# Kernel optimization log

Measured on AMD Instinct MI355X. Metric: run time of the kernel, lower is better.

## Reference

```python
import jax, jax.numpy as jnp
import numpy as np
import math

SEQ = 45000
FEAT = 30
DEPTH, HEADS, DK, MLP, C = 4, 4, 32, 512, 32
MAXSEQ = 512


def pos_embed_table():
    # Enformer-style basis functions over distances [-SEQ+1, SEQ-1]
    d = jnp.arange(-SEQ + 1, SEQ, dtype=jnp.float32)
    a = jnp.abs(d)[:, None]
    nb = FEAT // 6  # basis per class (exponential / central-mask / gamma)
    # exponential decay
    hl = 2.0 ** jnp.linspace(3.0, math.log(SEQ) / math.log(2.0), nb)
    e1 = jnp.exp(-math.log(2.0) / hl[None, :] * a)
    # central mask
    cw = 2.0 ** jnp.arange(1, nb + 1, dtype=jnp.float32) - 1.0
    e2 = (cw[None, :] > a).astype(jnp.float32)
    # gamma pdf
    stddev = SEQ / (2 * nb)
    start_mean = SEQ / nb
    mean = jnp.linspace(start_mean, float(SEQ), nb)
    conc = (mean / stddev) ** 2
    rate = mean / stddev ** 2
    logp = jax.scipy.special.xlogy(conc - 1.0, a) - rate * a
    logz = jax.scipy.special.gammaln(conc) - conc * jnp.log(rate)
    p = jnp.exp(logp - logz) + 1e-8
    e3 = p / jnp.max(p)
    e = jnp.concatenate([e1, e2, e3], axis=-1)
    return jnp.concatenate([e, jnp.sign(d)[:, None] * e], axis=-1)  # [2*SEQ-1, FEAT]


def layernorm(x, g, b, eps=1e-5):
    mu = jnp.mean(x, axis=-1, keepdims=True)
    var = jnp.var(x, axis=-1, keepdims=True)
    return (x - mu) * jax.lax.rsqrt(var + eps) * g + b


def setup_inputs() -> dict:
    key = jax.random.key(0)
    ks = jax.random.split(key, 16)
    B, L = 2, SEQ
    HD = HEADS * DK
    s = 0.02
    return {
        "x_skip": jax.random.normal(ks[0], (B, C, L), jnp.float32),
        "attention": jax.random.uniform(ks[1], (B, 3, L), jnp.float32),
        "ln1_g": jnp.ones((DEPTH, C), jnp.float32),
        "ln1_b": jnp.zeros((DEPTH, C), jnp.float32),
        "Wq": jax.random.normal(ks[2], (DEPTH, C, HD), jnp.float32) * s,
        "Wk": jax.random.normal(ks[3], (DEPTH, C, HD), jnp.float32) * s,
        "Wv": jax.random.normal(ks[4], (DEPTH, C, HD), jnp.float32) * s,
        "Wrel": jax.random.normal(ks[5], (DEPTH, FEAT, HD), jnp.float32) * s,
        "rcb": jax.random.normal(ks[6], (DEPTH, HEADS, DK), jnp.float32),
        "rpb": jax.random.normal(ks[7], (DEPTH, HEADS, DK), jnp.float32),
        "Wo": jax.random.normal(ks[8], (DEPTH, HD, C), jnp.float32) * s,
        "bo": jnp.zeros((DEPTH, C), jnp.float32),
        "ln2_g": jnp.ones((DEPTH, C), jnp.float32),
        "ln2_b": jnp.zeros((DEPTH, C), jnp.float32),
        "W1": jax.random.normal(ks[9], (DEPTH, C, MLP), jnp.float32) * s,
        "b1": jnp.zeros((DEPTH, MLP), jnp.float32),
        "W2": jax.random.normal(ks[10], (DEPTH, MLP, C), jnp.float32) * s,
        "b2": jnp.zeros((DEPTH, C), jnp.float32),
    }


def reference(x_skip, attention, ln1_g, ln1_b, Wq, Wk, Wv, Wrel, rcb, rpb, Wo, bo, ln2_g, ln2_b, W1, b1, W2, b2):
    B, Cc, L = x_skip.shape
    half = MAXSEQ // 2
    x_emb = jnp.swapaxes(x_skip, 1, 2)  # [B, L, C]
    # top splice sites by acceptor / donor score
    acc = jnp.argsort(-attention[:, 1, :], axis=1)[:, :half]
    don = jnp.argsort(-attention[:, 2, :], axis=1)[:, :half]
    idx = jnp.sort(jnp.concatenate([acc, don], axis=1), axis=1)  # [B, n]
    n = idx.shape[1]
    diff = idx[:, :, None] - idx[:, None, :] + SEQ - 1  # [B, n, n]
    positions = pos_embed_table()[diff]  # [B, n, n, FEAT]
    emb = jnp.take_along_axis(x_emb, idx[:, :, None], axis=1)  # [B, n, C]
    scale = DK ** -0.5
    for l in range(DEPTH):
        h = layernorm(emb, ln1_g[l], ln1_b[l])
        q = (h @ Wq[l]).reshape(B, n, HEADS, DK).transpose(0, 2, 1, 3) * scale
        k = (h @ Wk[l]).reshape(B, n, HEADS, DK).transpose(0, 2, 1, 3)
        v = (h @ Wv[l]).reshape(B, n, HEADS, DK).transpose(0, 2, 1, 3)
        content = jnp.einsum('bhid,bhjd->bhij', q + rcb[l][None, :, None, :], k)
        rel_k = (positions @ Wrel[l]).reshape(B, n, n, HEADS, DK)  # b i j h d
        rel = jnp.einsum('bhid,bijhd->bhij', q + rpb[l][None, :, None, :], rel_k)
        attn_w = jax.nn.softmax(content + rel, axis=-1)
        o = jnp.einsum('bhij,bhjd->bhid', attn_w, v)
        o = o.transpose(0, 2, 1, 3).reshape(B, n, HEADS * DK)
        emb = emb + o @ Wo[l] + bo[l]
        h2 = layernorm(emb, ln2_g[l], ln2_b[l])
        emb = emb + jax.nn.gelu(h2 @ W1[l] + b1[l], approximate=False) @ W2[l] + b2[l]
    out = jnp.zeros_like(x_emb).at[jnp.arange(B)[:, None], idx].set(emb)
    return jnp.swapaxes(out, 1, 2)  # [B, C, L]
```

## Files before the change

kernel.cpp:

```cpp
#include <hip/hip_runtime.h>
#include <math.h>

#define SEQL   45000
#define NBAT   2
#define CCH    32
#define NSEL   512
#define NHEAD  4
#define DKD    32
#define HDD    128
#define MLPD   512
#define CDCAP  2048
#define TKB    32
#define ETB    176

__device__ __forceinline__ unsigned short f2bf(float x) {
  unsigned u = __float_as_uint(x);
  u = (u + 0x7fffu + ((u >> 16) & 1u)) >> 16;
  return (unsigned short)u;
}
#define BFL(u) __uint_as_float((u) << 16)
#define BFH(u) __uint_as_float((u) & 0xffff0000u)
#define U8F(w, s) ((float)(((w) >> (s)) & 0xffu))

__global__ __launch_bounds__(256) void prep_kernel(const float* __restrict__ att,
                                                   unsigned char* __restrict__ E,
                                                   int* __restrict__ hist,
                                                   float* __restrict__ out) {
  {
    int nthr = gridDim.x * 256;
    int gt = blockIdx.x * 256 + threadIdx.x;
    float4 z4 = make_float4(0.f, 0.f, 0.f, 0.f);
    float4* o4 = (float4*)out;
    for (int i = gt; i < NBAT * CCH * SEQL / 4; i += nthr) o4[i] = z4;
  }
  if (blockIdx.x < ETB) {
    int a = blockIdx.x * 256 + threadIdx.x;
    if (a >= SEQL) return;
    float ad = (float)a;
    float outv[16];
    float log2S = log2f((float)SEQL);
    #pragma unroll
    for (int k = 0; k < 5; ++k) {
      float hl = exp2f(3.0f + (float)k * (log2S - 3.0f) * 0.25f);
      outv[k] = exp2f(-ad / hl);
    }
    const int cw[5] = {1, 3, 7, 15, 31};
    #pragma unroll
    for (int k = 0; k < 5; ++k) outv[5 + k] = (a < cw[k]) ? 1.0f : 0.0f;
    float pmax = 0.0f;
    float pk[5];
    #pragma unroll
    for (int k = 0; k < 5; ++k) {
      float mean = 9000.0f * (float)(k + 1);
      float sd = 4500.0f;
      float cc = (mean / sd) * (mean / sd);
      float rr = mean / (sd * sd);
      float logz = lgammaf(cc) - cc * logf(rr);
      float pp;
      if (a == 0) pp = 1e-8f;
      else pp = expf((cc - 1.0f) * logf(ad) - rr * ad - logz) + 1e-8f;
      pk[k] = pp;
      float mstar = (cc - 1.0f) / rr;
      float m0 = floorf(mstar), m1 = m0 + 1.0f;
      if (m1 > (float)(SEQL - 1)) m1 = (float)(SEQL - 1);
      float p0 = expf((cc - 1.0f) * logf(m0) - rr * m0 - logz) + 1e-8f;
      float p1 = expf((cc - 1.0f) * logf(m1) - rr * m1 - logz) + 1e-8f;
      pmax = fmaxf(pmax, fmaxf(p0, p1));
    }
    #pragma unroll
    for (int k = 0; k < 5; ++k) outv[10 + k] = pk[k] / pmax;
    outv[15] = 0.0f;
    unsigned by[16];
    #pragma unroll
    for (int k = 0; k < 15; ++k)
      by[k] = (unsigned)(fminf(fmaxf(outv[k], 0.f), 1.f) * 255.f + 0.5f);
    by[15] = 0u;
    uint4 o;
    o.x = by[0]  | (by[1]  << 8) | (by[2]  << 16) | (by[3]  << 24);
    o.y = by[4]  | (by[5]  << 8) | (by[6]  << 16) | (by[7]  << 24);
    o.z = by[8]  | (by[9]  << 8) | (by[10] << 16) | (by[11] << 24);
    o.w = by[12] | (by[13] << 8) | (by[14] << 16);
    *(uint4*)(E + (size_t)a * 16) = o;
  } else {
    int bid = blockIdx.x - ETB;
    int ch4 = bid / TKB;
    int blk = bid % TKB;
    int b = ch4 >> 1, ch = ch4 & 1;
    const float* row = att + ((size_t)b * 3 + 1 + ch) * SEQL;
    int* h = hist + (size_t)ch4 * 65536;
    int per = (SEQL + TKB - 1) / TKB;
    int lo = blk * per;
    int hi = lo + per; if (hi > SEQL) hi = SEQL;
    for (int i = lo + threadIdx.x; i < hi; i += 256)
      atomicAdd(&h[__float_as_uint(row[i]) >> 16], 1);
  }
}

__global__ __launch_bounds__(256) void topk_collect_kernel(
    const float* __restrict__ att, const int* __restrict__ hist,
    unsigned long long* __restrict__ cand, int* __restrict__ cnt) {
  __shared__ int s_scan[256];
  __shared__ int s_aux[2];
  int tid = threadIdx.x;
  int ch4 = blockIdx.x / TKB;
  int blk = blockIdx.x % TKB;
  const int* h = hist + (size_t)ch4 * 65536;
  {
    int base = tid * 256;
    int sum = 0;
    for (int i = 0; i < 64; ++i) {
      int4 v = ((const int4*)(h + base))[i];
      sum += v.x + v.y + v.z + v.w;
    }
    s_scan[tid] = sum;
  }
  __syncthreads();
  for (int d = 1; d < 256; d <<= 1) {
    int v = s_scan[tid] + ((tid + d < 256) ? s_scan[tid + d] : 0);
    __syncthreads();
    s_scan[tid] = v;
    __syncthreads();
  }
  {
    int sufEx = (tid == 255) ? 0 : s_scan[tid + 1];
    if (s_scan[tid] >= 256 && sufEx < 256) { s_aux[0] = tid; s_aux[1] = 256 - sufEx; }
  }
  __syncthreads();
  int chunk = s_aux[0], want = s_aux[1];
  s_scan[tid] = h[chunk * 256 + tid];
  __syncthreads();
  for (int d = 1; d < 256; d <<= 1) {
    int v = s_scan[tid] + ((tid + d < 256) ? s_scan[tid + d] : 0);
    __syncthreads();
    s_scan[tid] = v;
    __syncthreads();
  }
  {
    int sufEx2 = (tid == 255) ? 0 : s_scan[tid + 1];
    if (s_scan[tid] >= want && sufEx2 < want) s_aux[0] = chunk * 256 + tid;
  }
  __syncthreads();
  unsigned T16 = (unsigned)s_aux[0];
  int b = ch4 >> 1, ch = ch4 & 1;
  const float* row = att + ((size_t)b * 3 + 1 + ch) * SEQL;
  int per = (SEQL + TKB - 1) / TKB;
  int lo = blk * per;
  int hi = lo + per; if (hi > SEQL) hi = SEQL;
  for (int i = lo + tid; i < hi; i += 256) {
    unsigned key = __float_as_uint(row[i]);
    if ((key >> 16) >= T16) {
      int p = atomicAdd(&cnt[ch4], 1);
      if (p < CDCAP)
        cand[(size_t)ch4 * CDCAP + p] =
            ((unsigned long long)key << 32) | (unsigned)(~(unsigned)i);
    }
  }
}

__global__ __launch_bounds__(1024) void topk_sort_kernel(
    const unsigned long long* __restrict__ cand, const int* __restrict__ cnt,
    unsigned* __restrict__ chsel) {
  __shared__ unsigned long long sc[CDCAP];
  int ch4 = blockIdx.x, t = threadIdx.x;
  int n = cnt[ch4]; if (n > CDCAP) n = CDCAP;
  int P = 256;
  while (P < n) P <<= 1;
  for (int i = t; i < P; i += 1024)
    sc[i] = (i < n) ? cand[(size_t)ch4 * CDCAP + i] : 0ull;
  __syncthreads();
  for (int k = 2; k <= P; k <<= 1) {
    for (int j = k >> 1; j > 0; j >>= 1) {
      for (int i = t; i < P; i += 1024) {
        int ixj = i ^ j;
        if (ixj > i) {
          unsigned long long va = sc[i], vb2 = sc[ixj];
          bool up = ((i & k) == 0);
          if ((va < vb2) == up) { sc[i] = vb2; sc[ixj] = va; }
        }
      }
      __syncthreads();
    }
  }
  if (t < 256)
    chsel[(size_t)ch4 * 256 + t] = ~(unsigned)(sc[t] & 0xFFFFFFFFull);
}

__global__ __launch_bounds__(512) void topk_merge_kernel(const unsigned* __restrict__ chsel,
                                                         int* __restrict__ idx) {
  __shared__ int m[512];
  int b = blockIdx.x, tid = threadIdx.x;
  m[tid] = (int)chsel[(size_t)b * 512 + tid];
  __syncthreads();
  for (int k = 2; k <= 512; k <<= 1) {
    for (int j = k >> 1; j > 0; j >>= 1) {
      int ixj = tid ^ j;
      if (ixj > tid) {
        int va = m[tid], vb2 = m[ixj];
        bool up = ((tid & k) == 0);
        if ((va > vb2) == up) { m[tid] = vb2; m[ixj] = va; }
      }
      __syncthreads();
    }
  }
  idx[b * 512 + tid] = m[tid];
}

__global__ __launch_bounds__(128) void gqkv0_kernel(
    const float* __restrict__ x, const int* __restrict__ idx,
    const float* __restrict__ ln_g, const float* __restrict__ ln_b,
    const float* __restrict__ Wq, const float* __restrict__ Wk,
    const float* __restrict__ Wv, const float* __restrict__ Wrel,
    const float* __restrict__ rcb, const float* __restrict__ rpb,
    float* __restrict__ emb, float* __restrict__ qc,
    unsigned short* __restrict__ kbT, unsigned short* __restrict__ vT,
    float* __restrict__ wb) {
  __shared__ float qs[128];
  const int l = 0;
  int hd = threadIdx.x;
  int hh = hd >> 5, d = hd & 31;
  int row = blockIdx.x;
  int b = row >> 9, ii = row & 511;
  int li = idx[b * NSEL + ii];
  float h[32];
  float mu = 0.f;
  #pragma unroll
  for (int c = 0; c < 32; ++c) {
    h[c] = x[((size_t)b * CCH + c) * SEQL + li];
    mu += h[c];
  }
  if (hd < 32) emb[(size_t)row * CCH + hd] = h[hd];
  mu *= (1.0f / 32.0f);
  float var = 0.f;
  #pragma unroll
  for (int c = 0; c < 32; ++c) { float dd0 = h[c] - mu; var += dd0 * dd0; }
  var *= (1.0f / 32.0f);
  float rstd = rsqrtf(var + 1e-5f);
  const float* g = ln_g + l * CCH;
  const float* bb = ln_b + l * CCH;
  #pragma unroll
  for (int c = 0; c < 32; ++c) h[c] = (h[c] - mu) * rstd * g[c] + bb[c];
  const float* wq = Wq + (size_t)l * CCH * HDD + hd;
  const float* wk = Wk + (size_t)l * CCH * HDD + hd;
  const float* wv = Wv + (size_t)l * CCH * HDD + hd;
  float q = 0.f, kk = 0.f, vv = 0.f;
  #pragma unroll
  for (int c = 0; c < 32; ++c) {
    q += h[c] * wq[c * HDD];
    kk += h[c] * wk[c * HDD];
    vv += h[c] * wv[c * HDD];
  }
  q *= 0.17677669529663687f;
  qs[hd] = q;
  qc[(size_t)row * HDD + hd] = q + rcb[(l * NHEAD + hh) * DKD + d];
  size_t tpos = ((size_t)(b * 4 + hh) * 4 + (d >> 3)) * 4096 + (size_t)ii * 8 + (d & 7);
  kbT[tpos] = f2bf(kk);
  vT[tpos]  = f2bf(vv);
  __syncthreads();
  if (hd < 120) {
    int h2 = hd / 30, f = hd % 30;
    const float* wr = Wrel + ((size_t)l * 30 + f) * HDD + h2 * DKD;
    const float* rp = rpb + (l * NHEAD + h2) * DKD;
    const float* qsh = qs + h2 * DKD;
    float acc = 0.f;
    #pragma unroll
    for (int dd = 0; dd < 32; ++dd) acc += (qsh[dd] + rp[dd]) * wr[dd];
    wb[((size_t)row * NHEAD + h2) * 32 + f] = acc;
  }
}

__global__ __launch_bounds__(256, 4) void attn_kernel(
    const float* __restrict__ qc, const unsigned short* __restrict__ kbT,
    const unsigned short* __restrict__ vT, const float* __restrict__ wbuf,
    const unsigned char* __restrict__ E, const int* __restrict__ idx,
    float* __restrict__ ob) {
  __shared__ int idxl[512];
  int bid = blockIdx.x;
  int b = bid >> 9;
  int h = (bid >> 7) & 3;
  int i0 = (bid & 127) * 4;
  int tid = threadIdx.x;
  int wv = tid >> 6, ln = tid & 63;
  for (int i = tid; i < 512; i += 256) idxl[i] = idx[b * NSEL + i];
  __syncthreads();
  int i = i0 + wv;
  const float* qrow = qc + (size_t)(b * NSEL + i) * HDD + h * DKD;
  float q[32];
  #pragma unroll
  for (int d4 = 0; d4 < 8; ++d4) {
    float4 qv = *(const float4*)(qrow + d4 * 4);
    q[d4 * 4 + 0] = qv.x; q[d4 * 4 + 1] = qv.y;
    q[d4 * 4 + 2] = qv.z; q[d4 * 4 + 3] = qv.w;
  }
  const float* wrow = wbuf + ((size_t)(b * NSEL + i) * NHEAD + h) * 32;
  float w0[15], w1[15];
  #pragma unroll
  for (int f = 0; f < 15; ++f) {
    w0[f] = wrow[f] * (1.0f / 255.0f);
    w1[f] = wrow[15 + f] * (1.0f / 255.0f);
  }
  int ii = idxl[i];
  const uint4* kb4 = (const uint4*)kbT + (size_t)(b * 4 + h) * 4 * 512;
  const uint4* vb4 = (const uint4*)vT + (size_t)(b * 4 + h) * 4 * 512;
  float lg[8];
  #pragma unroll
  for (int u = 0; u < 8; ++u) {
    int j = u * 64 + ln;
    int dj = ii - idxl[j];
    float cacc = 0.f;
    #pragma unroll
    for (int dp = 0; dp < 4; ++dp) {
      uint4 kv = kb4[dp * 512 + j];
      cacc += q[dp * 8 + 0] * BFL(kv.x) + q[dp * 8 + 1] * BFH(kv.x)
            + q[dp * 8 + 2] * BFL(kv.y) + q[dp * 8 + 3] * BFH(kv.y)
            + q[dp * 8 + 4] * BFL(kv.z) + q[dp * 8 + 5] * BFH(kv.z)
            + q[dp * 8 + 6] * BFL(kv.w) + q[dp * 8 + 7] * BFH(kv.w);
    }
    int a = dj < 0 ? -dj : dj;
    uint4 e = *(const uint4*)(E + (size_t)a * 16);
    float r0 = U8F(e.x, 0)  * w0[0]  + U8F(e.x, 8)  * w0[1]
             + U8F(e.x, 16) * w0[2]  + U8F(e.x, 24) * w0[3]
             + U8F(e.y, 0)  * w0[4]  + U8F(e.y, 8)  * w0[5]
             + U8F(e.y, 16) * w0[6]  + U8F(e.y, 24) * w0[7]
             + U8F(e.z, 0)  * w0[8]  + U8F(e.z, 8)  * w0[9]
             + U8F(e.z, 16) * w0[10] + U8F(e.z, 24) * w0[11]
             + U8F(e.w, 0)  * w0[12] + U8F(e.w, 8)  * w0[13]
             + U8F(e.w, 16) * w0[14];
    float r1 = U8F(e.x, 0)  * w1[0]  + U8F(e.x, 8)  * w1[1]
             + U8F(e.x, 16) * w1[2]  + U8F(e.x, 24) * w1[3]
             + U8F(e.y, 0)  * w1[4]  + U8F(e.y, 8)  * w1[5]
             + U8F(e.y, 16) * w1[6]  + U8F(e.y, 24) * w1[7]
             + U8F(e.z, 0)  * w1[8]  + U8F(e.z, 8)  * w1[9]
             + U8F(e.z, 16) * w1[10] + U8F(e.z, 24) * w1[11]
             + U8F(e.w, 0)  * w1[12] + U8F(e.w, 8)  * w1[13]
             + U8F(e.w, 16) * w1[14];
    float sgn = dj > 0 ? 1.f : (dj < 0 ? -1.f : 0.f);
    lg[u] = cacc + r0 + sgn * r1;
  }
  float m = lg[0];
  #pragma unroll
  for (int u = 1; u < 8; ++u) m = fmaxf(m, lg[u]);
  #pragma unroll
  for (int s = 1; s < 64; s <<= 1) m = fmaxf(m, __shfl_xor(m, s));
  float ssum = 0.f;
  #pragma unroll
  for (int u = 0; u < 8; ++u) { lg[u] = __expf(lg[u] - m); ssum += lg[u]; }
  #pragma unroll
  for (int s = 1; s < 64; s <<= 1) ssum += __shfl_xor(ssum, s);
  float invs = 1.0f / ssum;
  float* obrow = ob + (size_t)(b * NSEL + i) * HDD + h * DKD;
  #pragma unroll
  for (int dp = 0; dp < 4; ++dp) {
    float acc[8] = {0.f, 0.f, 0.f, 0.f, 0.f, 0.f, 0.f, 0.f};
    #pragma unroll
    for (int u = 0; u < 8; ++u) {
      uint4 vv = vb4[dp * 512 + u * 64 + ln];
      float p = lg[u];
      acc[0] += p * BFL(vv.x); acc[1] += p * BFH(vv.x);
      acc[2] += p * BFL(vv.y); acc[3] += p * BFH(vv.y);
      acc[4] += p * BFL(vv.z); acc[5] += p * BFH(vv.z);
      acc[6] += p * BFL(vv.w); acc[7] += p * BFH(vv.w);
    }
    #pragma unroll
    for (int s = 1; s < 8; s <<= 1) {
      #pragma unroll
      for (int t = 0; t < 8; ++t) acc[t] += __shfl_xor(acc[t], s);
    }
    int sel = ln & 7;
    float y = acc[0];
    #pragma unroll
    for (int t = 1; t < 8; ++t) y = (sel == t) ? acc[t] : y;
    #pragma unroll
    for (int s = 8; s < 64; s <<= 1) y += __shfl_xor(y, s);
    if (ln < 8) obrow[dp * 8 + ln] = y * invs;
  }
}

__global__ __launch_bounds__(256) void mlpqkv_kernel(
    const float* __restrict__ ob, const float* __restrict__ Wo,
    const float* __restrict__ bo,
    const float* __restrict__ ln2_g, const float* __restrict__ ln2_b,
    const float* __restrict__ W1, const float* __restrict__ b1,
    const float* __restrict__ W2, const float* __restrict__ b2,
    const float* __restrict__ ln1_g, const float* __restrict__ ln1_b,
    const float* __restrict__ Wq, const float* __restrict__ Wk,
    const float* __restrict__ Wv, const float* __restrict__ Wrel,
    const float* __restrict__ rcb, const float* __restrict__ rpb,
    const int* __restrict__ idx, float* __restrict__ emb,
    float* __restrict__ qc, unsigned short* __restrict__ kbT,
    unsigned short* __restrict__ vT, float* __restrict__ wb,
    float* __restrict__ out, int layer) {
  __shared__ float part[8][32];
  __shared__ float res[32];
  __shared__ float hln[32];
  __shared__ float fin[32];
  __shared__ float a1s[MLPD];
  __shared__ float qs[128];
  int row = blockIdx.x;
  int b = row >> 9, ii = row & 511;
  int tid = threadIdx.x;
  int c = tid & 31, seg = tid >> 5;
  const float* wo = Wo + (size_t)layer * HDD * CCH + c;
  const float* orow = ob + (size_t)row * HDD;
  float pacc = 0.f;
  #pragma unroll
  for (int k = 0; k < 16; ++k) {
    int kk = seg * 16 + k;
    pacc += orow[kk] * wo[kk * CCH];
  }
  part[seg][c] = pacc;
  __syncthreads();
  if (tid < 32) {
    float s = bo[layer * CCH + tid] + emb[(size_t)row * CCH + tid];
    #pragma unroll
    for (int sg = 0; sg < 8; ++sg) s += part[sg][tid];
    res[tid] = s;
  }
  __syncthreads();
  if (tid < 32) {
    float mu = 0.f, s2 = 0.f;
    #pragma unroll
    for (int c2 = 0; c2 < 32; ++c2) { float v = res[c2]; mu += v; s2 += v * v; }
    mu *= (1.0f / 32.0f);
    float var = s2 * (1.0f / 32.0f) - mu * mu;
    float rstd = rsqrtf(var + 1e-5f);
    hln[tid] = (res[tid] - mu) * rstd * ln2_g[layer * CCH + tid] + ln2_b[layer * CCH + tid];
  }
  __syncthreads();
  const float* w1 = W1 + (size_t)layer * CCH * MLPD;
  float accA = b1[layer * MLPD + tid];
  float accB = b1[layer * MLPD + tid + 256];
  for (int c2 = 0; c2 < 32; ++c2) {
    float hv = hln[c2];
    accA += hv * w1[c2 * MLPD + tid];
    accB += hv * w1[c2 * MLPD + tid + 256];
  }
  a1s[tid]       = 0.5f * accA * (1.0f + erff(accA * 0.70710678118654752f));
  a1s[tid + 256] = 0.5f * accB * (1.0f + erff(accB * 0.70710678118654752f));
  __syncthreads();
  const float* w2 = W2 + (size_t)layer * MLPD * CCH;
  float acc2 = 0.f;
  #pragma unroll 4
  for (int mi = 0; mi < 64; ++mi) {
    int m = seg * 64 + mi;
    acc2 += a1s[m] * w2[m * CCH + c];
  }
  __syncthreads();
  part[seg][c] = acc2;
  __syncthreads();
  if (tid < 32) {
    float s = b2[layer * CCH + tid] + res[tid];
    #pragma unroll
    for (int sg = 0; sg < 8; ++sg) s += part[sg][tid];
    fin[tid] = s;
    if (layer < 3) emb[(size_t)row * CCH + tid] = s;
  }
  __syncthreads();
  if (layer == 3) {
    if (tid < 32) {
      int li = idx[b * NSEL + ii];
      out[((size_t)b * CCH + tid) * SEQL + li] = fin[tid];
    }
    return;
  }
  const int l1 = layer + 1;
  bool act = tid < 128;
  int hd = tid & 127;
  int hh = hd >> 5, d = hd & 31;
  if (act) {
    float h[32];
    float mu = 0.f;
    #pragma unroll
    for (int c2 = 0; c2 < 32; ++c2) { h[c2] = fin[c2]; mu += h[c2]; }
    mu *= (1.0f / 32.0f);
    float var = 0.f;
    #pragma unroll
    for (int c2 = 0; c2 < 32; ++c2) { float dd = h[c2] - mu; var += dd * dd; }
    var *= (1.0f / 32.0f);
    float rstd = rsqrtf(var + 1e-5f);
    const float* g = ln1_g + l1 * CCH;
    const float* bb = ln1_b + l1 * CCH;
    #pragma unroll
    for (int c2 = 0; c2 < 32; ++c2) h[c2] = (h[c2] - mu) * rstd * g[c2] + bb[c2];
    const float* wq = Wq + (size_t)l1 * CCH * HDD + hd;
    const float* wk = Wk + (size_t)l1 * CCH * HDD + hd;
    const float* wv = Wv + (size_t)l1 * CCH * HDD + hd;
    float q = 0.f, kk = 0.f, vv = 0.f;
    #pragma unroll
    for (int c2 = 0; c2 < 32; ++c2) {
      q += h[c2] * wq[c2 * HDD];
      kk += h[c2] * wk[c2 * HDD];
      vv += h[c2] * wv[c2 * HDD];
    }
    q *= 0.17677669529663687f;
    qs[hd] = q;
    qc[(size_t)row * HDD + hd] = q + rcb[(l1 * NHEAD + hh) * DKD + d];
    size_t tpos = ((size_t)(b * 4 + hh) * 4 + (d >> 3)) * 4096 + (size_t)ii * 8 + (d & 7);
    kbT[tpos] = f2bf(kk);
    vT[tpos]  = f2bf(vv);
  }
  __syncthreads();
  if (act && hd < 120) {
    int h2 = hd / 30, f = hd % 30;
    const float* rp = rpb + (l1 * NHEAD + h2) * DKD;
    const float* wr = Wrel + ((size_t)l1 * 30 + f) * HDD + h2 * DKD;
    const float* qsh = qs + h2 * DKD;
    float acc = 0.f;
    #pragma unroll
    for (int dd = 0; dd < 32; ++dd) acc += (qsh[dd] + rp[dd]) * wr[dd];
    wb[((size_t)row * NHEAD + h2) * 32 + f] = acc;
  }
}

extern "C" void kernel_launch(void* const* d_in, const int* in_sizes, int n_in,
                              void* d_out, int out_size, void* d_ws, size_t ws_size,
                              hipStream_t stream) {
  (void)in_sizes; (void)n_in; (void)ws_size; (void)out_size;
  const float* x_skip    = (const float*)d_in[0];
  const float* attention = (const float*)d_in[1];
  const float* ln1_g = (const float*)d_in[2];
  const float* ln1_b = (const float*)d_in[3];
  const float* Wq    = (const float*)d_in[4];
  const float* Wk    = (const float*)d_in[5];
  const float* Wv    = (const float*)d_in[6];
  const float* Wrel  = (const float*)d_in[7];
  const float* rcb   = (const float*)d_in[8];
  const float* rpb   = (const float*)d_in[9];
  const float* Wo    = (const float*)d_in[10];
  const float* bo    = (const float*)d_in[11];
  const float* ln2_g = (const float*)d_in[12];
  const float* ln2_b = (const float*)d_in[13];
  const float* W1    = (const float*)d_in[14];
  const float* b1    = (const float*)d_in[15];
  const float* W2    = (const float*)d_in[16];
  const float* b2    = (const float*)d_in[17];
  float* out = (float*)d_out;
  char* ws = (char*)d_ws;

  unsigned char* E = (unsigned char*)(ws + 0);
  int*      idx   = (int*)(ws + 1441792);
  float*    emb   = (float*)(ws + 1445888);
  float*    qc    = (float*)(ws + 1576960);
  unsigned short* kbT = (unsigned short*)(ws + 2101248);
  unsigned short* vT  = (unsigned short*)(ws + 2363392);
  float*    wb    = (float*)(ws + 2625536);
  float*    ob    = (float*)(ws + 3149824);
  int*      hist  = (int*)(ws + 3674112);
  int*      cnt   = (int*)(ws + 4722688);
  unsigned long long* cand = (unsigned long long*)(ws + 4722720);
  unsigned* chsel = (unsigned*)(ws + 4788256);

  hipMemsetAsync(ws + 3674112, 0, 1048576 + 32, stream);
  prep_kernel<<<ETB + 4 * TKB, 256, 0, stream>>>(attention, E, hist, out);
  topk_collect_kernel<<<4 * TKB, 256, 0, stream>>>(attention, hist, cand, cnt);
  topk_sort_kernel<<<4, 1024, 0, stream>>>(cand, cnt, chsel);
  topk_merge_kernel<<<2, 512, 0, stream>>>(chsel, idx);
  gqkv0_kernel<<<1024, 128, 0, stream>>>(x_skip, idx, ln1_g, ln1_b, Wq, Wk, Wv,
                                         Wrel, rcb, rpb, emb, qc, kbT, vT, wb);
  for (int l = 0; l < 4; ++l) {
    attn_kernel<<<1024, 256, 0, stream>>>(qc, kbT, vT, wb, E, idx, ob);
    mlpqkv_kernel<<<1024, 256, 0, stream>>>(ob, Wo, bo, ln2_g, ln2_b, W1, b1,
                                            W2, b2, ln1_g, ln1_b, Wq, Wk, Wv,
                                            Wrel, rcb, rpb, idx, emb, qc, kbT,
                                            vT, wb, out, l);
  }
}
```

Measured before the change: 322.0 us.

## Share relative-position basis gather across heads via shared memory per query row

Blocks are remapped so each block handles one query row with one wave per head, instead of four query rows for a single head. The gathered and unpacked position-basis values for every key (15 features plus sign) are computed once into shared memory and then reused by all four heads. Before, each head repeated the random E-table gather and the byte unpacking. The cost is 32 KB of shared memory per block, which may lower occupancy, plus a block-wide barrier.

```diff
diff --git a/kernel.cpp b/kernel.cpp
--- a/kernel.cpp
+++ b/kernel.cpp
@@ -273,16 +273,37 @@
     const unsigned short* __restrict__ vT, const float* __restrict__ wbuf,
     const unsigned char* __restrict__ E, const int* __restrict__ idx,
     float* __restrict__ ob) {
-  __shared__ int idxl[512];
+  __shared__ float es[16 * 512];
   int bid = blockIdx.x;
   int b = bid >> 9;
-  int h = (bid >> 7) & 3;
-  int i0 = (bid & 127) * 4;
+  int i = bid & 511;
   int tid = threadIdx.x;
-  int wv = tid >> 6, ln = tid & 63;
-  for (int i = tid; i < 512; i += 256) idxl[i] = idx[b * NSEL + i];
-  __syncthreads();
-  int i = i0 + wv;
+  int ii = idx[b * NSEL + i];
+  #pragma unroll
+  for (int rep = 0; rep < 2; ++rep) {
+    int j = tid + rep * 256;
+    int dj = ii - idx[b * NSEL + j];
+    int a = dj < 0 ? -dj : dj;
+    uint4 e = *(const uint4*)(E + (size_t)a * 16);
+    es[0  * 512 + j] = U8F(e.x, 0);
+    es[1  * 512 + j] = U8F(e.x, 8);
+    es[2  * 512 + j] = U8F(e.x, 16);
+    es[3  * 512 + j] = U8F(e.x, 24);
+    es[4  * 512 + j] = U8F(e.y, 0);
+    es[5  * 512 + j] = U8F(e.y, 8);
+    es[6  * 512 + j] = U8F(e.y, 16);
+    es[7  * 512 + j] = U8F(e.y, 24);
+    es[8  * 512 + j] = U8F(e.z, 0);
+    es[9  * 512 + j] = U8F(e.z, 8);
+    es[10 * 512 + j] = U8F(e.z, 16);
+    es[11 * 512 + j] = U8F(e.z, 24);
+    es[12 * 512 + j] = U8F(e.w, 0);
+    es[13 * 512 + j] = U8F(e.w, 8);
+    es[14 * 512 + j] = U8F(e.w, 16);
+    es[15 * 512 + j] = dj > 0 ? 1.f : (dj < 0 ? -1.f : 0.f);
+  }
+  __syncthreads();
+  int h = tid >> 6, ln = tid & 63;
   const float* qrow = qc + (size_t)(b * NSEL + i) * HDD + h * DKD;
   float q[32];
   #pragma unroll
@@ -298,14 +319,12 @@
     w0[f] = wrow[f] * (1.0f / 255.0f);
     w1[f] = wrow[15 + f] * (1.0f / 255.0f);
   }
-  int ii = idxl[i];
   const uint4* kb4 = (const uint4*)kbT + (size_t)(b * 4 + h) * 4 * 512;
   const uint4* vb4 = (const uint4*)vT + (size_t)(b * 4 + h) * 4 * 512;
   float lg[8];
   #pragma unroll
   for (int u = 0; u < 8; ++u) {
     int j = u * 64 + ln;
-    int dj = ii - idxl[j];
     float cacc = 0.f;
     #pragma unroll
     for (int dp = 0; dp < 4; ++dp) {
@@ -315,26 +334,14 @@
             + q[dp * 8 + 4] * BFL(kv.z) + q[dp * 8 + 5] * BFH(kv.z)
             + q[dp * 8 + 6] * BFL(kv.w) + q[dp * 8 + 7] * BFH(kv.w);
     }
-    int a = dj < 0 ? -dj : dj;
-    uint4 e = *(const uint4*)(E + (size_t)a * 16);
-    float r0 = U8F(e.x, 0)  * w0[0]  + U8F(e.x, 8)  * w0[1]
-             + U8F(e.x, 16) * w0[2]  + U8F(e.x, 24) * w0[3]
-             + U8F(e.y, 0)  * w0[4]  + U8F(e.y, 8)  * w0[5]
-             + U8F(e.y, 16) * w0[6]  + U8F(e.y, 24) * w0[7]
-             + U8F(e.z, 0)  * w0[8]  + U8F(e.z, 8)  * w0[9]
-             + U8F(e.z, 16) * w0[10] + U8F(e.z, 24) * w0[11]
-             + U8F(e.w, 0)  * w0[12] + U8F(e.w, 8)  * w0[13]
-             + U8F(e.w, 16) * w0[14];
-    float r1 = U8F(e.x, 0)  * w1[0]  + U8F(e.x, 8)  * w1[1]
-             + U8F(e.x, 16) * w1[2]  + U8F(e.x, 24) * w1[3]
-             + U8F(e.y, 0)  * w1[4]  + U8F(e.y, 8)  * w1[5]
-             + U8F(e.y, 16) * w1[6]  + U8F(e.y, 24) * w1[7]
-             + U8F(e.z, 0)  * w1[8]  + U8F(e.z, 8)  * w1[9]
-             + U8F(e.z, 16) * w1[10] + U8F(e.z, 24) * w1[11]
-             + U8F(e.w, 0)  * w1[12] + U8F(e.w, 8)  * w1[13]
-             + U8F(e.w, 16) * w1[14];
-    float sgn = dj > 0 ? 1.f : (dj < 0 ? -1.f : 0.f);
-    lg[u] = cacc + r0 + sgn * r1;
+    float r0 = 0.f, r1 = 0.f;
+    #pragma unroll
+    for (int f = 0; f < 15; ++f) {
+      float ef = es[f * 512 + j];
+      r0 += ef * w0[f];
+      r1 += ef * w1[f];
+    }
+    lg[u] = cacc + r0 + es[15 * 512 + j] * r1;
   }
   float m = lg[0];
   #pragma unroll
```

Measured after the change: 325.0 us. Within noise of the previous version (+0.9%).
